# Performance work log

Measured on AMD Instinct MI355X. Metric: run time of the kernel, lower is better.

## Reference

```python
import jax, jax.numpy as jnp
import numpy as np

N = 50000      # nodes
E = 800000     # edges (before self-loops)
IN = 128       # in_channels
HID = 64       # hidden_channels
HEADS = 4      # num_heads of gat1
ACT = 5        # num_actions
NEG_SLOPE = 0.2


def gat_conv(x, edge_index, W, a_src, a_dst, bias, heads, out_ch):
    """PyG-style GATConv (concat=True, add_self_loops=True, eval mode)."""
    n = x.shape[0]
    loops = jnp.arange(n)
    src = jnp.concatenate([edge_index[0], loops])  # messages flow src -> dst
    dst = jnp.concatenate([edge_index[1], loops])
    h = (x @ W).reshape(n, heads, out_ch)                 # [N,H,C]
    alpha_src = jnp.sum(h * a_src, axis=-1)               # [N,H]
    alpha_dst = jnp.sum(h * a_dst, axis=-1)               # [N,H]
    e = jax.nn.leaky_relu(alpha_src[src] + alpha_dst[dst], NEG_SLOPE)  # [Et,H]
    # numerically-stable segment softmax over incoming edges of each dst node
    e_max = jax.lax.stop_gradient(jax.ops.segment_max(e, dst, num_segments=n))
    e_max = jnp.where(jnp.isfinite(e_max), e_max, 0.0)
    p = jnp.exp(e - e_max[dst])                           # [Et,H]
    denom = jax.ops.segment_sum(p, dst, num_segments=n)   # [N,H]
    alpha = p / (denom[dst] + 1e-16)                      # [Et,H]
    out = jax.ops.segment_sum(h[src] * alpha[:, :, None], dst, num_segments=n)
    return out.reshape(n, heads * out_ch) + bias


def setup_inputs() -> dict:
    key = jax.random.key(0)
    ks = jax.random.split(key, 12)
    s = 0.1
    return {
        "x": jax.random.normal(ks[0], (N, IN), jnp.float32),
        "edge_index": jax.random.randint(ks[1], (2, E), 0, N, dtype=jnp.int32),
        "W1": jax.random.normal(ks[2], (IN, HEADS * HID), jnp.float32) * s,
        "a1_src": jax.random.normal(ks[3], (HEADS, HID), jnp.float32) * s,
        "a1_dst": jax.random.normal(ks[4], (HEADS, HID), jnp.float32) * s,
        "b1": jnp.zeros((HEADS * HID,), jnp.float32),
        "W2": jax.random.normal(ks[5], (HEADS * HID, HID), jnp.float32) * s,
        "a2_src": jax.random.normal(ks[6], (1, HID), jnp.float32) * s,
        "a2_dst": jax.random.normal(ks[7], (1, HID), jnp.float32) * s,
        "b2": jnp.zeros((HID,), jnp.float32),
        "Wfc": jax.random.normal(ks[8], (HID, ACT), jnp.float32) * s,
        "bfc": jnp.zeros((ACT,), jnp.float32),
    }


def reference(x, edge_index, W1, a1_src, a1_dst, b1, W2, a2_src, a2_dst, b2, Wfc, bfc):
    # x.view(-1, F) is a no-op for already-flat [N, F] input; dropout skipped (eval).
    h = jax.nn.relu(gat_conv(x, edge_index, W1, a1_src, a1_dst, b1, HEADS, HID))
    h = jax.nn.relu(gat_conv(h, edge_index, W2, a2_src, a2_dst, b2, 1, HID))
    return h @ Wfc + bfc  # [N, num_actions]
```

## Files before the change

kernel.cpp:

```cpp
#include <hip/hip_runtime.h>

#define NEG_SLOPE 0.2f

__device__ __forceinline__ float leaky(float x) { return x > 0.f ? x : NEG_SLOPE * x; }

__device__ __forceinline__ void unpack2(unsigned u, float& lo, float& hi) {
    union { unsigned u; float f; } a, b;
    a.u = u << 16; b.u = u & 0xffff0000u;
    lo = a.f; hi = b.f;
}

__device__ __forceinline__ unsigned short f2bf(float f) {
    unsigned u = __float_as_uint(f);
    u += 0x7fffu + ((u >> 16) & 1u);
    return (unsigned short)(u >> 16);
}

__global__ void k_count(const int* __restrict__ dst, int E, int* __restrict__ cnt) {
    int i = blockIdx.x * blockDim.x + threadIdx.x;
    if (i < E) atomicAdd(&cnt[dst[i]], 1);
}

__global__ __launch_bounds__(256) void k_scanA(const int* __restrict__ cnt, int* __restrict__ rowptr,
                                               int* __restrict__ bsum, int n) {
    int b = blockIdx.x, t = threadIdx.x;
    int lane = t & 63, w = t >> 6;
    int i0 = b * 1024 + t * 4;
    int v0 = (i0 + 0 < n) ? cnt[i0 + 0] : 0;
    int v1 = (i0 + 1 < n) ? cnt[i0 + 1] : 0;
    int v2 = (i0 + 2 < n) ? cnt[i0 + 2] : 0;
    int v3 = (i0 + 3 < n) ? cnt[i0 + 3] : 0;
    int r0 = v0, r1 = r0 + v1, r2 = r1 + v2, r3 = r2 + v3;
    int s = r3;
    int q = s;
    #pragma unroll
    for (int off = 1; off < 64; off <<= 1) {
        int tval = __shfl_up(q, off);
        if (lane >= off) q += tval;
    }
    __shared__ int wsum[4];
    if (lane == 63) wsum[w] = q;
    __syncthreads();
    int woff = 0;
    #pragma unroll
    for (int k = 0; k < 4; k++) if (k < w) woff += wsum[k];
    int excl = woff + q - s;
    if (i0 + 0 < n) rowptr[1 + i0 + 0] = excl + r0;
    if (i0 + 1 < n) rowptr[1 + i0 + 1] = excl + r1;
    if (i0 + 2 < n) rowptr[1 + i0 + 2] = excl + r2;
    if (i0 + 3 < n) rowptr[1 + i0 + 3] = excl + r3;
    if (t == 255) bsum[b] = woff + q;
}

__global__ void k_scanB(const int* __restrict__ bsum, int* __restrict__ bscan, int nb) {
    int lane = threadIdx.x & 63;
    int v = (lane < nb) ? bsum[lane] : 0;
    #pragma unroll
    for (int off = 1; off < 64; off <<= 1) {
        int t = __shfl_up(v, off);
        if (lane >= off) v += t;
    }
    if (lane < nb) bscan[lane] = v;
}

__global__ __launch_bounds__(256) void k_scanC(int* __restrict__ rowptr, const int* __restrict__ bscan, int n) {
    int b = blockIdx.x, t = threadIdx.x;
    int i0 = b * 1024 + t * 4;
    if (b == 0) {
        if (t == 0) rowptr[0] = 0;
        return;
    }
    int add = bscan[b - 1];
    #pragma unroll
    for (int j = 0; j < 4; j++)
        if (i0 + j < n) rowptr[1 + i0 + j] += add;
}

__global__ void k_copy(const int* __restrict__ src, int* __restrict__ dst, int n) {
    int i = blockIdx.x * blockDim.x + threadIdx.x;
    if (i < n) dst[i] = src[i];
}

__global__ void k_scatter(const int* __restrict__ srcn, const int* __restrict__ dstn, int E,
                          int* __restrict__ wptr, int* __restrict__ col) {
    int i = blockIdx.x * blockDim.x + threadIdx.x;
    if (i < E) {
        int d = dstn[i];
        int pos = atomicAdd(&wptr[d], 1);
        col[pos] = srcn[i];
    }
}

template <int BMT, bool WF32, bool WBF16, bool FALPHA>
__global__ __launch_bounds__(256) void k_gemm(const float* __restrict__ A, const float* __restrict__ B,
                                              float* __restrict__ C, unsigned short* __restrict__ Cb,
                                              const float* __restrict__ a_s, const float* __restrict__ a_d,
                                              float* __restrict__ asrc, float* __restrict__ adst,
                                              int M, int N, int K) {
    constexpr int RT = BMT / 16;
    constexpr int APASS = BMT / 32;
    __shared__ float As[32][BMT + 4];
    __shared__ float Bs[32][68];
    int row0 = blockIdx.x * BMT, col0 = blockIdx.y * 64;
    int tid = threadIdx.x;
    int tx = tid & 15, ty = tid >> 4;
    float acc[RT][4] = {};
    for (int kk = 0; kk < K; kk += 32) {
        int ar = tid >> 3;
        int ac = (tid & 7) * 4;
        #pragma unroll
        for (int p = 0; p < APASS; p++) {
            int r = ar + p * 32;
            int gr = row0 + r;
            float4 v = make_float4(0.f, 0.f, 0.f, 0.f);
            if (gr < M) v = *reinterpret_cast<const float4*>(&A[(size_t)gr * K + kk + ac]);
            As[ac + 0][r] = v.x; As[ac + 1][r] = v.y;
            As[ac + 2][r] = v.z; As[ac + 3][r] = v.w;
        }
        int br = tid >> 4;
        int bc = (tid & 15) * 4;
        #pragma unroll
        for (int p = 0; p < 2; p++) {
            int r = br + p * 16;
            float4 v = *reinterpret_cast<const float4*>(&B[(size_t)(kk + r) * N + col0 + bc]);
            *reinterpret_cast<float4*>(&Bs[r][bc]) = v;
        }
        __syncthreads();
        #pragma unroll
        for (int k = 0; k < 32; k++) {
            float a[RT];
            #pragma unroll
            for (int i = 0; i < RT; i += 4) {
                float4 av = *reinterpret_cast<const float4*>(&As[k][ty * RT + i]);
                a[i + 0] = av.x; a[i + 1] = av.y; a[i + 2] = av.z; a[i + 3] = av.w;
            }
            float4 bv = *reinterpret_cast<const float4*>(&Bs[k][tx * 4]);
            float b[4] = {bv.x, bv.y, bv.z, bv.w};
            #pragma unroll
            for (int i = 0; i < RT; i++)
                #pragma unroll
                for (int j = 0; j < 4; j++) acc[i][j] = fmaf(a[i], b[j], acc[i][j]);
        }
        __syncthreads();
    }
    float4 as4, ad4;
    if (FALPHA) {
        as4 = *reinterpret_cast<const float4*>(&a_s[col0 + tx * 4]);
        ad4 = *reinterpret_cast<const float4*>(&a_d[col0 + tx * 4]);
    }
    int HV = N >> 6, hd = col0 >> 6;
    #pragma unroll
    for (int i = 0; i < RT; i++) {
        int gr = row0 + ty * RT + i;
        if (gr < M) {
            if (WF32) {
                float4 v = make_float4(acc[i][0], acc[i][1], acc[i][2], acc[i][3]);
                *reinterpret_cast<float4*>(&C[(size_t)gr * N + col0 + tx * 4]) = v;
            }
            if (WBF16) {
                ushort4 u;
                u.x = f2bf(acc[i][0]); u.y = f2bf(acc[i][1]);
                u.z = f2bf(acc[i][2]); u.w = f2bf(acc[i][3]);
                *reinterpret_cast<ushort4*>(&Cb[(size_t)gr * N + col0 + tx * 4]) = u;
            }
            if (FALPHA) {
                float ps = acc[i][0] * as4.x + acc[i][1] * as4.y + acc[i][2] * as4.z + acc[i][3] * as4.w;
                float pd = acc[i][0] * ad4.x + acc[i][1] * ad4.y + acc[i][2] * ad4.z + acc[i][3] * ad4.w;
                #pragma unroll
                for (int off = 1; off <= 8; off <<= 1) { ps += __shfl_xor(ps, off); pd += __shfl_xor(pd, off); }
                if (tx == 0) { asrc[(size_t)gr * HV + hd] = ps; adst[(size_t)gr * HV + hd] = pd; }
            }
        }
    }
}

__global__ __launch_bounds__(256) void k_agg1(const unsigned short* __restrict__ hb,
                                              const float* __restrict__ asrc, const float* __restrict__ adst,
                                              const int* __restrict__ rowptr, const int* __restrict__ col,
                                              const float* __restrict__ bias, float* __restrict__ out, int n) {
    int node = blockIdx.x;
    int t = threadIdx.x, hd = t >> 6, l = t & 63;
    int rep = l >> 3, q = l & 7;
    int base = rowptr[node], deg = rowptr[node + 1] - base;
    float adst_n = adst[node * 4 + hd];
    float p_self = __expf(leaky(asrc[node * 4 + hd] + adst_n));
    float acc[8] = {};
    float dsum = 0.f;
    if (rep == 0) {
        uint4 u = *reinterpret_cast<const uint4*>(&hb[(size_t)node * 256 + hd * 64 + q * 8]);
        float f[8];
        unpack2(u.x, f[0], f[1]); unpack2(u.y, f[2], f[3]);
        unpack2(u.z, f[4], f[5]); unpack2(u.w, f[6], f[7]);
        #pragma unroll
        for (int j = 0; j < 8; j++) acc[j] = p_self * f[j];
        dsum = p_self;
    }

    for (int c0 = 0; c0 < deg; c0 += 16) {
        int ia = c0 + rep, ib = ia + 8;
        bool va = ia < deg, vb = ib < deg;
        int sa = 0, sb = 0;
        if (va) sa = col[base + ia];
        if (vb) sb = col[base + ib];
        uint4 ua = make_uint4(0, 0, 0, 0), ub = make_uint4(0, 0, 0, 0);
        if (va) ua = *reinterpret_cast<const uint4*>(&hb[(size_t)sa * 256 + hd * 64 + q * 8]);
        if (vb) ub = *reinterpret_cast<const uint4*>(&hb[(size_t)sb * 256 + hd * 64 + q * 8]);
        float pa = 0.f, pb = 0.f;
        if (va) pa = __expf(leaky(asrc[sa * 4 + hd] + adst_n));
        if (vb) pb = __expf(leaky(asrc[sb * 4 + hd] + adst_n));
        float f[8];
        unpack2(ua.x, f[0], f[1]); unpack2(ua.y, f[2], f[3]);
        unpack2(ua.z, f[4], f[5]); unpack2(ua.w, f[6], f[7]);
        #pragma unroll
        for (int j = 0; j < 8; j++) acc[j] = fmaf(pa, f[j], acc[j]);
        unpack2(ub.x, f[0], f[1]); unpack2(ub.y, f[2], f[3]);
        unpack2(ub.z, f[4], f[5]); unpack2(ub.w, f[6], f[7]);
        #pragma unroll
        for (int j = 0; j < 8; j++) acc[j] = fmaf(pb, f[j], acc[j]);
        dsum += pa + pb;
    }
    #pragma unroll
    for (int off = 8; off <= 32; off <<= 1) {
        #pragma unroll
        for (int j = 0; j < 8; j++) acc[j] += __shfl_xor(acc[j], off);
        dsum += __shfl_xor(dsum, off);
    }
    if (rep == 0) {
        float inv = 1.f / (dsum + 1e-16f);
        float r[8];
        #pragma unroll
        for (int j = 0; j < 8; j++) r[j] = fmaxf(acc[j] * inv + bias[hd * 64 + q * 8 + j], 0.f);
        float4 v0 = make_float4(r[0], r[1], r[2], r[3]);
        float4 v1 = make_float4(r[4], r[5], r[6], r[7]);
        *reinterpret_cast<float4*>(&out[(size_t)node * 256 + hd * 64 + q * 8]) = v0;
        *reinterpret_cast<float4*>(&out[(size_t)node * 256 + hd * 64 + q * 8 + 4]) = v1;
    }
}

__global__ __launch_bounds__(256) void k_agg2fc(const unsigned short* __restrict__ hb,
                                                const float* __restrict__ asrc, const float* __restrict__ adst,
                                                const int* __restrict__ rowptr, const int* __restrict__ col,
                                                const float* __restrict__ bias, const float* __restrict__ Wfc,
                                                const float* __restrict__ bfc, float* __restrict__ out, int n) {
    int node = blockIdx.x * 4 + (threadIdx.x >> 6);
    int l = threadIdx.x & 63;
    if (node >= n) return;
    int rep = l >> 3, q = l & 7;
    int base = rowptr[node], deg = rowptr[node + 1] - base;
    float adst_n = adst[node];
    float p_self = __expf(leaky(asrc[node] + adst_n));
    float acc[8] = {};
    float dsum = 0.f;
    if (rep == 0) {
        uint4 u = *reinterpret_cast<const uint4*>(&hb[(size_t)node * 64 + q * 8]);
        float f[8];
        unpack2(u.x, f[0], f[1]); unpack2(u.y, f[2], f[3]);
        unpack2(u.z, f[4], f[5]); unpack2(u.w, f[6], f[7]);
        #pragma unroll
        for (int j = 0; j < 8; j++) acc[j] = p_self * f[j];
        dsum = p_self;
    }

    for (int c0 = 0; c0 < deg; c0 += 16) {
        int ia = c0 + rep, ib = ia + 8;
        bool va = ia < deg, vb = ib < deg;
        int sa = 0, sb = 0;
        if (va) sa = col[base + ia];
        if (vb) sb = col[base + ib];
        uint4 ua = make_uint4(0, 0, 0, 0), ub = make_uint4(0, 0, 0, 0);
        if (va) ua = *reinterpret_cast<const uint4*>(&hb[(size_t)sa * 64 + q * 8]);
        if (vb) ub = *reinterpret_cast<const uint4*>(&hb[(size_t)sb * 64 + q * 8]);
        float pa = 0.f, pb = 0.f;
        if (va) pa = __expf(leaky(asrc[sa] + adst_n));
        if (vb) pb = __expf(leaky(asrc[sb] + adst_n));
        float f[8];
        unpack2(ua.x, f[0], f[1]); unpack2(ua.y, f[2], f[3]);
        unpack2(ua.z, f[4], f[5]); unpack2(ua.w, f[6], f[7]);
        #pragma unroll
        for (int j = 0; j < 8; j++) acc[j] = fmaf(pa, f[j], acc[j]);
        unpack2(ub.x, f[0], f[1]); unpack2(ub.y, f[2], f[3]);
        unpack2(ub.z, f[4], f[5]); unpack2(ub.w, f[6], f[7]);
        #pragma unroll
        for (int j = 0; j < 8; j++) acc[j] = fmaf(pb, f[j], acc[j]);
        dsum += pa + pb;
    }
    #pragma unroll
    for (int off = 8; off <= 32; off <<= 1) {
        #pragma unroll
        for (int j = 0; j < 8; j++) acc[j] += __shfl_xor(acc[j], off);
        dsum += __shfl_xor(dsum, off);
    }
    float inv = 1.f / (dsum + 1e-16f);
    float r[8];
    #pragma unroll
    for (int j = 0; j < 8; j++) r[j] = fmaxf(acc[j] * inv + bias[q * 8 + j], 0.f);
    #pragma unroll
    for (int a = 0; a < 5; a++) {
        float part = 0.f;
        #pragma unroll
        for (int j = 0; j < 8; j++) part = fmaf(r[j], Wfc[(q * 8 + j) * 5 + a], part);
        #pragma unroll
        for (int off = 1; off <= 4; off <<= 1) part += __shfl_xor(part, off);
        if (l == 0) out[(size_t)node * 5 + a] = part + bfc[a];
    }
}

extern "C" void kernel_launch(void* const* d_in, const int* in_sizes, int n_in,
                              void* d_out, int out_size, void* d_ws, size_t ws_size,
                              hipStream_t stream) {
    const float* x   = (const float*)d_in[0];
    const int*   ei  = (const int*)d_in[1];
    const float* W1  = (const float*)d_in[2];
    const float* a1s = (const float*)d_in[3];
    const float* a1d = (const float*)d_in[4];
    const float* b1  = (const float*)d_in[5];
    const float* W2  = (const float*)d_in[6];
    const float* a2s = (const float*)d_in[7];
    const float* a2d = (const float*)d_in[8];
    const float* b2  = (const float*)d_in[9];
    const float* Wfc = (const float*)d_in[10];
    const float* bfc = (const float*)d_in[11];
    float* out = (float*)d_out;

    int n = in_sizes[0] / 128;
    int E = in_sizes[1] / 2;
    const int* srcn = ei;
    const int* dstn = ei + E;

    char* ws = (char*)d_ws;
    size_t off = 0;
    auto alloc = [&](size_t bytes) -> void* {
        void* p = ws + off;
        off += (bytes + 255) & ~(size_t)255;
        return p;
    };
    unsigned short* h1b = (unsigned short*)alloc((size_t)n * 256 * 2);
    float* out1   = (float*)alloc((size_t)n * 256 * 4);
    unsigned short* h2b = (unsigned short*)alloc((size_t)n * 64 * 2);
    float* asrc1  = (float*)alloc((size_t)n * 4 * 4);
    float* adst1  = (float*)alloc((size_t)n * 4 * 4);
    int*   rowptr = (int*)alloc((size_t)(n + 1) * 4);
    int*   wptr   = (int*)alloc((size_t)n * 4);
    int*   col    = (int*)alloc((size_t)E * 4);
    int*   bsum   = (int*)alloc(64 * 4);
    int*   bscan  = (int*)alloc(64 * 4);
    float* asrc2 = asrc1;
    float* adst2 = adst1;

    int nb = (n + 1023) / 1024;

    hipMemsetAsync(wptr, 0, (size_t)n * 4, stream);
    k_count<<<(E + 255) / 256, 256, 0, stream>>>(dstn, E, wptr);
    k_scanA<<<nb, 256, 0, stream>>>(wptr, rowptr, bsum, n);
    k_scanB<<<1, 64, 0, stream>>>(bsum, bscan, nb);
    k_scanC<<<nb, 256, 0, stream>>>(rowptr, bscan, n);
    k_copy<<<(n + 255) / 256, 256, 0, stream>>>(rowptr, wptr, n);
    k_scatter<<<(E + 255) / 256, 256, 0, stream>>>(srcn, dstn, E, wptr, col);

    k_gemm<128, false, true, true><<<dim3((n + 127) / 128, 4), 256, 0, stream>>>(
        x, W1, nullptr, h1b, a1s, a1d, asrc1, adst1, n, 256, 128);
    k_agg1<<<n, 256, 0, stream>>>(h1b, asrc1, adst1, rowptr, col, b1, out1, n);
    k_gemm<64, false, true, true><<<dim3((n + 63) / 64, 1), 256, 0, stream>>>(
        out1, W2, nullptr, h2b, a2s, a2d, asrc2, adst2, n, 64, 256);
    k_agg2fc<<<(n + 3) / 4, 256, 0, stream>>>(h2b, asrc2, adst2, rowptr, col, b2, Wfc, bfc, out, n);
}
```

Before: 495.2 us.

## Add padded ELL neighbor table for first 32 edges in aggregation kernels

Builds a fixed-width ELL table (32 slots per node, -1 padded) during the CSR scatter. Both aggregation kernels then load all first-32 neighbors in one vectorized int4 read and issue four independent feature gathers per lane up front, with no per-chunk loop. Only nodes with degree above 32 fall back to the CSR loop. This is meant to raise memory-level parallelism and cut loop and branch overhead for average degree ~16. It costs an extra 6.4MB memset and more scatter writes, and nodes with few neighbors now do redundant gathers of node 0.

```diff
diff --git a/kernel.cpp b/kernel.cpp
--- a/kernel.cpp
+++ b/kernel.cpp
@@ -1,6 +1,7 @@
 #include <hip/hip_runtime.h>
 
 #define NEG_SLOPE 0.2f
+#define ELLW 32
 
 __device__ __forceinline__ float leaky(float x) { return x > 0.f ? x : NEG_SLOPE * x; }
 
@@ -82,12 +83,16 @@
 }
 
 __global__ void k_scatter(const int* __restrict__ srcn, const int* __restrict__ dstn, int E,
-                          int* __restrict__ wptr, int* __restrict__ col) {
+                          const int* __restrict__ rowptr, int* __restrict__ wptr,
+                          int* __restrict__ col, int* __restrict__ ell) {
     int i = blockIdx.x * blockDim.x + threadIdx.x;
     if (i < E) {
         int d = dstn[i];
+        int s = srcn[i];
         int pos = atomicAdd(&wptr[d], 1);
-        col[pos] = srcn[i];
+        col[pos] = s;
+        int slot = pos - rowptr[d];
+        if (slot < ELLW) ell[(size_t)d * ELLW + slot] = s;
     }
 }
 
@@ -176,48 +181,82 @@
 
 __global__ __launch_bounds__(256) void k_agg1(const unsigned short* __restrict__ hb,
                                               const float* __restrict__ asrc, const float* __restrict__ adst,
-                                              const int* __restrict__ rowptr, const int* __restrict__ col,
-                                              const float* __restrict__ bias, float* __restrict__ out, int n) {
+                                              const int* __restrict__ rowptr, const int* __restrict__ ell,
+                                              const int* __restrict__ col, const float* __restrict__ bias,
+                                              float* __restrict__ out, int n) {
     int node = blockIdx.x;
     int t = threadIdx.x, hd = t >> 6, l = t & 63;
     int rep = l >> 3, q = l & 7;
-    int base = rowptr[node], deg = rowptr[node + 1] - base;
     float adst_n = adst[node * 4 + hd];
     float p_self = __expf(leaky(asrc[node * 4 + hd] + adst_n));
+
+    int4 cv = *reinterpret_cast<const int4*>(&ell[(size_t)node * ELLW + rep * 4]);
+    int s0 = cv.x, s1 = cv.y, s2 = cv.z, s3 = cv.w;
+    bool v0 = s0 >= 0, v1 = s1 >= 0, v2 = s2 >= 0, v3 = s3 >= 0;
+    s0 = v0 ? s0 : 0; s1 = v1 ? s1 : 0; s2 = v2 ? s2 : 0; s3 = v3 ? s3 : 0;
+    uint4 u0 = *reinterpret_cast<const uint4*>(&hb[(size_t)s0 * 256 + hd * 64 + q * 8]);
+    uint4 u1 = *reinterpret_cast<const uint4*>(&hb[(size_t)s1 * 256 + hd * 64 + q * 8]);
+    uint4 u2 = *reinterpret_cast<const uint4*>(&hb[(size_t)s2 * 256 + hd * 64 + q * 8]);
+    uint4 u3 = *reinterpret_cast<const uint4*>(&hb[(size_t)s3 * 256 + hd * 64 + q * 8]);
+    float e0 = asrc[s0 * 4 + hd], e1 = asrc[s1 * 4 + hd];
+    float e2 = asrc[s2 * 4 + hd], e3 = asrc[s3 * 4 + hd];
+    float p0 = v0 ? __expf(leaky(e0 + adst_n)) : 0.f;
+    float p1 = v1 ? __expf(leaky(e1 + adst_n)) : 0.f;
+    float p2 = v2 ? __expf(leaky(e2 + adst_n)) : 0.f;
+    float p3 = v3 ? __expf(leaky(e3 + adst_n)) : 0.f;
+
     float acc[8] = {};
-    float dsum = 0.f;
+    float dsum = p0 + p1 + p2 + p3;
     if (rep == 0) {
-        uint4 u = *reinterpret_cast<const uint4*>(&hb[(size_t)node * 256 + hd * 64 + q * 8]);
+        uint4 un = *reinterpret_cast<const uint4*>(&hb[(size_t)node * 256 + hd * 64 + q * 8]);
         float f[8];
-        unpack2(u.x, f[0], f[1]); unpack2(u.y, f[2], f[3]);
-        unpack2(u.z, f[4], f[5]); unpack2(u.w, f[6], f[7]);
+        unpack2(un.x, f[0], f[1]); unpack2(un.y, f[2], f[3]);
+        unpack2(un.z, f[4], f[5]); unpack2(un.w, f[6], f[7]);
         #pragma unroll
         for (int j = 0; j < 8; j++) acc[j] = p_self * f[j];
-        dsum = p_self;
-    }
-
-    for (int c0 = 0; c0 < deg; c0 += 16) {
-        int ia = c0 + rep, ib = ia + 8;
-        bool va = ia < deg, vb = ib < deg;
-        int sa = 0, sb = 0;
-        if (va) sa = col[base + ia];
-        if (vb) sb = col[base + ib];
-        uint4 ua = make_uint4(0, 0, 0, 0), ub = make_uint4(0, 0, 0, 0);
-        if (va) ua = *reinterpret_cast<const uint4*>(&hb[(size_t)sa * 256 + hd * 64 + q * 8]);
-        if (vb) ub = *reinterpret_cast<const uint4*>(&hb[(size_t)sb * 256 + hd * 64 + q * 8]);
-        float pa = 0.f, pb = 0.f;
-        if (va) pa = __expf(leaky(asrc[sa * 4 + hd] + adst_n));
-        if (vb) pb = __expf(leaky(asrc[sb * 4 + hd] + adst_n));
+        dsum += p_self;
+    }
+    {
         float f[8];
-        unpack2(ua.x, f[0], f[1]); unpack2(ua.y, f[2], f[3]);
-        unpack2(ua.z, f[4], f[5]); unpack2(ua.w, f[6], f[7]);
-        #pragma unroll
-        for (int j = 0; j < 8; j++) acc[j] = fmaf(pa, f[j], acc[j]);
-        unpack2(ub.x, f[0], f[1]); unpack2(ub.y, f[2], f[3]);
-        unpack2(ub.z, f[4], f[5]); unpack2(ub.w, f[6], f[7]);
-        #pragma unroll
-        for (int j = 0; j < 8; j++) acc[j] = fmaf(pb, f[j], acc[j]);
-        dsum += pa + pb;
+        unpack2(u0.x, f[0], f[1]); unpack2(u0.y, f[2], f[3]);
+        unpack2(u0.z, f[4], f[5]); unpack2(u0.w, f[6], f[7]);
+        #pragma unroll
+        for (int j = 0; j < 8; j++) acc[j] = fmaf(p0, f[j], acc[j]);
+        unpack2(u1.x, f[0], f[1]); unpack2(u1.y, f[2], f[3]);
+        unpack2(u1.z, f[4], f[5]); unpack2(u1.w, f[6], f[7]);
+        #pragma unroll
+        for (int j = 0; j < 8; j++) acc[j] = fmaf(p1, f[j], acc[j]);
+        unpack2(u2.x, f[0], f[1]); unpack2(u2.y, f[2], f[3]);
+        unpack2(u2.z, f[4], f[5]); unpack2(u2.w, f[6], f[7]);
+        #pragma unroll
+        for (int j = 0; j < 8; j++) acc[j] = fmaf(p2, f[j], acc[j]);
+        unpack2(u3.x, f[0], f[1]); unpack2(u3.y, f[2], f[3]);
+        unpack2(u3.z, f[4], f[5]); unpack2(u3.w, f[6], f[7]);
+        #pragma unroll
+        for (int j = 0; j < 8; j++) acc[j] = fmaf(p3, f[j], acc[j]);
+    }
+    int base = rowptr[node], deg = rowptr[node + 1] - base;
+    if (deg > ELLW) {
+        for (int c0 = ELLW; c0 < deg; c0 += 16) {
+            int ia = c0 + rep, ib = ia + 8;
+            bool va = ia < deg, vb = ib < deg;
+            int sa = va ? col[base + ia] : 0;
+            int sb = vb ? col[base + ib] : 0;
+            uint4 ua = *reinterpret_cast<const uint4*>(&hb[(size_t)sa * 256 + hd * 64 + q * 8]);
+            uint4 ub = *reinterpret_cast<const uint4*>(&hb[(size_t)sb * 256 + hd * 64 + q * 8]);
+            float pa = va ? __expf(leaky(asrc[sa * 4 + hd] + adst_n)) : 0.f;
+            float pb = vb ? __expf(leaky(asrc[sb * 4 + hd] + adst_n)) : 0.f;
+            float f[8];
+            unpack2(ua.x, f[0], f[1]); unpack2(ua.y, f[2], f[3]);
+            unpack2(ua.z, f[4], f[5]); unpack2(ua.w, f[6], f[7]);
+            #pragma unroll
+            for (int j = 0; j < 8; j++) acc[j] = fmaf(pa, f[j], acc[j]);
+            unpack2(ub.x, f[0], f[1]); unpack2(ub.y, f[2], f[3]);
+            unpack2(ub.z, f[4], f[5]); unpack2(ub.w, f[6], f[7]);
+            #pragma unroll
+            for (int j = 0; j < 8; j++) acc[j] = fmaf(pb, f[j], acc[j]);
+            dsum += pa + pb;
+        }
     }
     #pragma unroll
     for (int off = 8; off <= 32; off <<= 1) {
@@ -230,59 +269,92 @@
         float r[8];
         #pragma unroll
         for (int j = 0; j < 8; j++) r[j] = fmaxf(acc[j] * inv + bias[hd * 64 + q * 8 + j], 0.f);
-        float4 v0 = make_float4(r[0], r[1], r[2], r[3]);
-        float4 v1 = make_float4(r[4], r[5], r[6], r[7]);
-        *reinterpret_cast<float4*>(&out[(size_t)node * 256 + hd * 64 + q * 8]) = v0;
-        *reinterpret_cast<float4*>(&out[(size_t)node * 256 + hd * 64 + q * 8 + 4]) = v1;
+        float4 w0 = make_float4(r[0], r[1], r[2], r[3]);
+        float4 w1 = make_float4(r[4], r[5], r[6], r[7]);
+        *reinterpret_cast<float4*>(&out[(size_t)node * 256 + hd * 64 + q * 8]) = w0;
+        *reinterpret_cast<float4*>(&out[(size_t)node * 256 + hd * 64 + q * 8 + 4]) = w1;
     }
 }
 
 __global__ __launch_bounds__(256) void k_agg2fc(const unsigned short* __restrict__ hb,
                                                 const float* __restrict__ asrc, const float* __restrict__ adst,
-                                                const int* __restrict__ rowptr, const int* __restrict__ col,
-                                                const float* __restrict__ bias, const float* __restrict__ Wfc,
-                                                const float* __restrict__ bfc, float* __restrict__ out, int n) {
+                                                const int* __restrict__ rowptr, const int* __restrict__ ell,
+                                                const int* __restrict__ col, const float* __restrict__ bias,
+                                                const float* __restrict__ Wfc, const float* __restrict__ bfc,
+                                                float* __restrict__ out, int n) {
     int node = blockIdx.x * 4 + (threadIdx.x >> 6);
     int l = threadIdx.x & 63;
     if (node >= n) return;
     int rep = l >> 3, q = l & 7;
-    int base = rowptr[node], deg = rowptr[node + 1] - base;
     float adst_n = adst[node];
     float p_self = __expf(leaky(asrc[node] + adst_n));
+
+    int4 cv = *reinterpret_cast<const int4*>(&ell[(size_t)node * ELLW + rep * 4]);
+    int s0 = cv.x, s1 = cv.y, s2 = cv.z, s3 = cv.w;
+    bool v0 = s0 >= 0, v1 = s1 >= 0, v2 = s2 >= 0, v3 = s3 >= 0;
+    s0 = v0 ? s0 : 0; s1 = v1 ? s1 : 0; s2 = v2 ? s2 : 0; s3 = v3 ? s3 : 0;
+    uint4 u0 = *reinterpret_cast<const uint4*>(&hb[(size_t)s0 * 64 + q * 8]);
+    uint4 u1 = *reinterpret_cast<const uint4*>(&hb[(size_t)s1 * 64 + q * 8]);
+    uint4 u2 = *reinterpret_cast<const uint4*>(&hb[(size_t)s2 * 64 + q * 8]);
+    uint4 u3 = *reinterpret_cast<const uint4*>(&hb[(size_t)s3 * 64 + q * 8]);
+    float e0 = asrc[s0], e1 = asrc[s1], e2 = asrc[s2], e3 = asrc[s3];
+    float p0 = v0 ? __expf(leaky(e0 + adst_n)) : 0.f;
+    float p1 = v1 ? __expf(leaky(e1 + adst_n)) : 0.f;
+    float p2 = v2 ? __expf(leaky(e2 + adst_n)) : 0.f;
+    float p3 = v3 ? __expf(leaky(e3 + adst_n)) : 0.f;
+
     float acc[8] = {};
-    float dsum = 0.f;
+    float dsum = p0 + p1 + p2 + p3;
     if (rep == 0) {
-        uint4 u = *reinterpret_cast<const uint4*>(&hb[(size_t)node * 64 + q * 8]);
+        uint4 un = *reinterpret_cast<const uint4*>(&hb[(size_t)node * 64 + q * 8]);
         float f[8];
-        unpack2(u.x, f[0], f[1]); unpack2(u.y, f[2], f[3]);
-        unpack2(u.z, f[4], f[5]); unpack2(u.w, f[6], f[7]);
+        unpack2(un.x, f[0], f[1]); unpack2(un.y, f[2], f[3]);
+        unpack2(un.z, f[4], f[5]); unpack2(un.w, f[6], f[7]);
         #pragma unroll
         for (int j = 0; j < 8; j++) acc[j] = p_self * f[j];
-        dsum = p_self;
-    }
-
-    for (int c0 = 0; c0 < deg; c0 += 16) {
-        int ia = c0 + rep, ib = ia + 8;
-        bool va = ia < deg, vb = ib < deg;
-        int sa = 0, sb = 0;
-        if (va) sa = col[base + ia];
-        if (vb) sb = col[base + ib];
-        uint4 ua = make_uint4(0, 0, 0, 0), ub = make_uint4(0, 0, 0, 0);
-        if (va) ua = *reinterpret_cast<const uint4*>(&hb[(size_t)sa * 64 + q * 8]);
-        if (vb) ub = *reinterpret_cast<const uint4*>(&hb[(size_t)sb * 64 + q * 8]);
-        float pa = 0.f, pb = 0.f;
-        if (va) pa = __expf(leaky(asrc[sa] + adst_n));
-        if (vb) pb = __expf(leaky(asrc[sb] + adst_n));
+        dsum += p_self;
+    }
+    {
         float f[8];
-        unpack2(ua.x, f[0], f[1]); unpack2(ua.y, f[2], f[3]);
-        unpack2(ua.z, f[4], f[5]); unpack2(ua.w, f[6], f[7]);
-        #pragma unroll
-        for (int j = 0; j < 8; j++) acc[j] = fmaf(pa, f[j], acc[j]);
-        unpack2(ub.x, f[0], f[1]); unpack2(ub.y, f[2], f[3]);
-        unpack2(ub.z, f[4], f[5]); unpack2(ub.w, f[6], f[7]);
-        #pragma unroll
-        for (int j = 0; j < 8; j++) acc[j] = fmaf(pb, f[j], acc[j]);
-        dsum += pa + pb;
+        unpack2(u0.x, f[0], f[1]); unpack2(u0.y, f[2], f[3]);
+        unpack2(u0.z, f[4], f[5]); unpack2(u0.w, f[6], f[7]);
+        #pragma unroll
+        for (int j = 0; j < 8; j++) acc[j] = fmaf(p0, f[j], acc[j]);
+        unpack2(u1.x, f[0], f[1]); unpack2(u1.y, f[2], f[3]);
+        unpack2(u1.z, f[4], f[5]); unpack2(u1.w, f[6], f[7]);
+        #pragma unroll
+        for (int j = 0; j < 8; j++) acc[j] = fmaf(p1, f[j], acc[j]);
+        unpack2(u2.x, f[0], f[1]); unpack2(u2.y, f[2], f[3]);
+        unpack2(u2.z, f[4], f[5]); unpack2(u2.w, f[6], f[7]);
+        #pragma unroll
+        for (int j = 0; j < 8; j++) acc[j] = fmaf(p2, f[j], acc[j]);
+        unpack2(u3.x, f[0], f[1]); unpack2(u3.y, f[2], f[3]);
+        unpack2(u3.z, f[4], f[5]); unpack2(u3.w, f[6], f[7]);
+        #pragma unroll
+        for (int j = 0; j < 8; j++) acc[j] = fmaf(p3, f[j], acc[j]);
+    }
+    int base = rowptr[node], deg = rowptr[node + 1] - base;
+    if (deg > ELLW) {
+        for (int c0 = ELLW; c0 < deg; c0 += 16) {
+            int ia = c0 + rep, ib = ia + 8;
+            bool va = ia < deg, vb = ib < deg;
+            int sa = va ? col[base + ia] : 0;
+            int sb = vb ? col[base + ib] : 0;
+            uint4 ua = *reinterpret_cast<const uint4*>(&hb[(size_t)sa * 64 + q * 8]);
+            uint4 ub = *reinterpret_cast<const uint4*>(&hb[(size_t)sb * 64 + q * 8]);
+            float pa = va ? __expf(leaky(asrc[sa] + adst_n)) : 0.f;
+            float pb = vb ? __expf(leaky(asrc[sb] + adst_n)) : 0.f;
+            float f[8];
+            unpack2(ua.x, f[0], f[1]); unpack2(ua.y, f[2], f[3]);
+            unpack2(ua.z, f[4], f[5]); unpack2(ua.w, f[6], f[7]);
+            #pragma unroll
+            for (int j = 0; j < 8; j++) acc[j] = fmaf(pa, f[j], acc[j]);
+            unpack2(ub.x, f[0], f[1]); unpack2(ub.y, f[2], f[3]);
+            unpack2(ub.z, f[4], f[5]); unpack2(ub.w, f[6], f[7]);
+            #pragma unroll
+            for (int j = 0; j < 8; j++) acc[j] = fmaf(pb, f[j], acc[j]);
+            dsum += pa + pb;
+        }
     }
     #pragma unroll
     for (int off = 8; off <= 32; off <<= 1) {
@@ -342,6 +414,7 @@
     int*   rowptr = (int*)alloc((size_t)(n + 1) * 4);
     int*   wptr   = (int*)alloc((size_t)n * 4);
     int*   col    = (int*)alloc((size_t)E * 4);
+    int*   ell    = (int*)alloc((size_t)n * ELLW * 4);
     int*   bsum   = (int*)alloc(64 * 4);
     int*   bscan  = (int*)alloc(64 * 4);
     float* asrc2 = asrc1;
@@ -350,17 +423,18 @@
     int nb = (n + 1023) / 1024;
 
     hipMemsetAsync(wptr, 0, (size_t)n * 4, stream);
+    hipMemsetAsync(ell, 0xFF, (size_t)n * ELLW * 4, stream);
     k_count<<<(E + 255) / 256, 256, 0, stream>>>(dstn, E, wptr);
     k_scanA<<<nb, 256, 0, stream>>>(wptr, rowptr, bsum, n);
     k_scanB<<<1, 64, 0, stream>>>(bsum, bscan, nb);
     k_scanC<<<nb, 256, 0, stream>>>(rowptr, bscan, n);
     k_copy<<<(n + 255) / 256, 256, 0, stream>>>(rowptr, wptr, n);
-    k_scatter<<<(E + 255) / 256, 256, 0, stream>>>(srcn, dstn, E, wptr, col);
+    k_scatter<<<(E + 255) / 256, 256, 0, stream>>>(srcn, dstn, E, rowptr, wptr, col, ell);
 
     k_gemm<128, false, true, true><<<dim3((n + 127) / 128, 4), 256, 0, stream>>>(
         x, W1, nullptr, h1b, a1s, a1d, asrc1, adst1, n, 256, 128);
-    k_agg1<<<n, 256, 0, stream>>>(h1b, asrc1, adst1, rowptr, col, b1, out1, n);
+    k_agg1<<<n, 256, 0, stream>>>(h1b, asrc1, adst1, rowptr, ell, col, b1, out1, n);
     k_gemm<64, false, true, true><<<dim3((n + 63) / 64, 1), 256, 0, stream>>>(
         out1, W2, nullptr, h2b, a2s, a2d, asrc2, adst2, n, 64, 256);
-    k_agg2fc<<<(n + 3) / 4, 256, 0, stream>>>(h2b, asrc2, adst2, rowptr, col, b2, Wfc, bfc, out, n);
-}
+    k_agg2fc<<<(n + 3) / 4, 256, 0, stream>>>(h2b, asrc2, adst2, rowptr, ell, col, b2, Wfc, bfc, out, n);
+}
```

After: 473.5 us. -4.4%, faster.
